# Performance work log

Hardware: AMD Instinct MI355X
Metric: run time of the kernel (lower is better)

The kernel has to match this reference:

```python
import jax, jax.numpy as jnp
import numpy as np

N, E, DIN, H, C = 50000, 800000, 128, 2, 64  # C = hidden_dim*heads (per-head out channels); concat=False -> mean over heads -> layer out dim C
NUM_CLASSES = 4
EPS_GN = 1e-5


def setup_inputs() -> dict:
    key = jax.random.key(0)

    def rn(i, shape, scale):
        return (jax.random.normal(jax.random.fold_in(key, i), shape) * scale).astype(jnp.float32)

    inp = {
        "x": rn(0, (N, DIN), 1.0),
        "edge_index": jax.random.randint(jax.random.fold_in(key, 1), (2, E), 0, N, dtype=jnp.int32),
    }
    layer_in = [DIN, C]
    for li, din in enumerate(layer_in, 1):
        s = 1.0 / np.sqrt(din)
        base = 10 * li
        inp[f"Wl{li}"] = rn(base + 0, (din, H * C), s)
        inp[f"bl{li}"] = jnp.zeros((H * C,), jnp.float32)
        inp[f"Wr{li}"] = rn(base + 1, (din, H * C), s)
        inp[f"br{li}"] = jnp.zeros((H * C,), jnp.float32)
        inp[f"att{li}"] = rn(base + 2, (H, C), 1.0 / np.sqrt(C))
        inp[f"bias{li}"] = jnp.zeros((C,), jnp.float32)
        inp[f"gng{li}"] = jnp.ones((C,), jnp.float32)   # GraphNorm weight
        inp[f"gnb{li}"] = jnp.zeros((C,), jnp.float32)  # GraphNorm bias
        inp[f"gna{li}"] = jnp.ones((C,), jnp.float32)   # GraphNorm mean_scale
    inp["W1"] = rn(100, (C, NUM_CLASSES), 1.0 / np.sqrt(C))
    inp["b1"] = jnp.zeros((NUM_CLASSES,), jnp.float32)
    return inp


def gatv2_layer(x, src, dst, Wl, bl, Wr, br, att, bias):
    # PyG GATv2Conv, concat=False. x: [N, din]
    n = x.shape[0]
    xl = (x @ Wl + bl).reshape(n, H, C)  # source transform
    xr = (x @ Wr + br).reshape(n, H, C)  # target transform
    m = jax.nn.leaky_relu(xl[src] + xr[dst], negative_slope=0.2)  # [E', H, C]
    e = jnp.einsum('ehc,hc->eh', m, att)                           # [E', H]
    emax = jax.lax.stop_gradient(jax.ops.segment_max(e, dst, num_segments=n))
    ee = jnp.exp(e - emax[dst])
    denom = jax.ops.segment_sum(ee, dst, num_segments=n)
    alpha = ee / (denom[dst] + 1e-16)                              # softmax over in-edges of each target
    out = jax.ops.segment_sum(alpha[:, :, None] * xl[src], dst, num_segments=n)  # [N, H, C]
    return out.mean(axis=1) + bias  # concat=False -> mean over heads


def graph_norm(x, gamma, beta, mean_scale):
    # single-graph GraphNorm: stats over all nodes, per feature
    mean = x.mean(axis=0, keepdims=True)
    xc = x - mean_scale * mean
    var = (xc * xc).mean(axis=0, keepdims=True)
    return gamma * xc * jax.lax.rsqrt(var + EPS_GN) + beta


def reference(x, edge_index,
              Wl1, bl1, Wr1, br1, att1, bias1, gng1, gnb1, gna1,
              Wl2, bl2, Wr2, br2, att2, bias2, gng2, gnb2, gna2,
              W1, b1):
    src, dst = edge_index[0], edge_index[1]
    loops = jnp.arange(N, dtype=src.dtype)  # add_self_loops=True
    src = jnp.concatenate([src, loops])
    dst = jnp.concatenate([dst, loops])

    h = gatv2_layer(x, src, dst, Wl1, bl1, Wr1, br1, att1, bias1)
    h = graph_norm(h, gng1, gnb1, gna1)
    h = gatv2_layer(h, src, dst, Wl2, bl2, Wr2, br2, att2, bias2)
    h = graph_norm(h, gng2, gnb2, gna2)

    logits = h @ W1 + b1  # dropout is identity in eval
    return jax.nn.log_softmax(logits, axis=1)
```

## Files before the change

kernel.cpp:

```cpp
#include <hip/hip_runtime.h>
#include <hip/hip_bf16.h>
#include <math.h>

#define HC   128
#define CCH  64
#define NBK  256

typedef __attribute__((ext_vector_type(8))) short short8;
typedef __attribute__((ext_vector_type(4))) float floatx4;

__device__ __forceinline__ unsigned short f2bf(float f) {
  unsigned u = __float_as_uint(f);
  u += 0x7fffu + ((u >> 16) & 1u);
  return (unsigned short)(u >> 16);
}

__device__ __forceinline__ void unpack8(uint4 u, float* f) {
  f[0] = __uint_as_float(u.x << 16);
  f[1] = __uint_as_float(u.x & 0xffff0000u);
  f[2] = __uint_as_float(u.y << 16);
  f[3] = __uint_as_float(u.y & 0xffff0000u);
  f[4] = __uint_as_float(u.z << 16);
  f[5] = __uint_as_float(u.z & 0xffff0000u);
  f[6] = __uint_as_float(u.w << 16);
  f[7] = __uint_as_float(u.w & 0xffff0000u);
}

template <int CTRL>
__device__ __forceinline__ float dpp_add(float x) {
  int t = __builtin_amdgcn_update_dpp(0, __float_as_int(x), CTRL, 0xf, 0xf, true);
  return x + __int_as_float(t);
}

template <int K>
__device__ __forceinline__ void gemm32rows(
    const unsigned short* __restrict__ A,
    const unsigned short* __restrict__ Wlt, const unsigned short* __restrict__ Wrt,
    const float* __restrict__ bl, const float* __restrict__ br,
    unsigned short* __restrict__ xlb, unsigned short* __restrict__ xrb,
    int M, int row0, int tid) {
  const int w = tid >> 6;
  const int lane = tid & 63;
  const bool isR = w >= 2;
  const unsigned short* Wt = isR ? Wrt : Wlt;
  const float* bias = isR ? br : bl;
  unsigned short* out = isR ? xrb : xlb;
  const int col0 = (w & 1) * 64;
  const int mrow = lane & 15, quad = lane >> 4;
  const unsigned short* pa0 = A + (size_t)(row0 + mrow) * K + quad * 8;
  const unsigned short* pa1 = pa0 + (size_t)16 * K;
  const unsigned short* pb = Wt + (size_t)(col0 + mrow) * K + quad * 8;
  floatx4 acc[2][4];
#pragma unroll
  for (int gp = 0; gp < 2; gp++)
#pragma unroll
    for (int ct = 0; ct < 4; ct++) acc[gp][ct] = (floatx4){0.f, 0.f, 0.f, 0.f};
#pragma unroll
  for (int k0 = 0; k0 < K; k0 += 32) {
    short8 a0 = *(const short8*)(pa0 + k0);
    short8 a1 = *(const short8*)(pa1 + k0);
    short8 b0 = *(const short8*)(pb + k0);
    short8 b1 = *(const short8*)(pb + 16 * K + k0);
    short8 b2 = *(const short8*)(pb + 32 * K + k0);
    short8 b3 = *(const short8*)(pb + 48 * K + k0);
    acc[0][0] = __builtin_amdgcn_mfma_f32_16x16x32_bf16(a0, b0, acc[0][0], 0, 0, 0);
    acc[1][0] = __builtin_amdgcn_mfma_f32_16x16x32_bf16(a1, b0, acc[1][0], 0, 0, 0);
    acc[0][1] = __builtin_amdgcn_mfma_f32_16x16x32_bf16(a0, b1, acc[0][1], 0, 0, 0);
    acc[1][1] = __builtin_amdgcn_mfma_f32_16x16x32_bf16(a1, b1, acc[1][1], 0, 0, 0);
    acc[0][2] = __builtin_amdgcn_mfma_f32_16x16x32_bf16(a0, b2, acc[0][2], 0, 0, 0);
    acc[1][2] = __builtin_amdgcn_mfma_f32_16x16x32_bf16(a1, b2, acc[1][2], 0, 0, 0);
    acc[0][3] = __builtin_amdgcn_mfma_f32_16x16x32_bf16(a0, b3, acc[0][3], 0, 0, 0);
    acc[1][3] = __builtin_amdgcn_mfma_f32_16x16x32_bf16(a1, b3, acc[1][3], 0, 0, 0);
  }
#pragma unroll
  for (int gp = 0; gp < 2; gp++) {
#pragma unroll
    for (int ct = 0; ct < 4; ct++) {
      int col = col0 + ct * 16 + mrow;
      float bv = bias[col];
#pragma unroll
      for (int r = 0; r < 4; r++) {
        int row = row0 + gp * 16 + quad * 4 + r;
        if (row < M) out[(size_t)row * HC + col] = f2bf(acc[gp][ct][r] + bv);
      }
    }
  }
}

__global__ __launch_bounds__(256) void bin_cast(
    const int* __restrict__ ei, int E, int chunk, int nB,
    int* __restrict__ blkCnt, int* __restrict__ bucketTotal,
    const float* __restrict__ x, unsigned short* __restrict__ xb, int cnt4,
    const float* __restrict__ Wl, const float* __restrict__ Wr,
    unsigned short* __restrict__ Wlt, unsigned short* __restrict__ Wrt) {
  if ((int)blockIdx.x < NBK) {
    __shared__ int cnt[512];
    for (int j = threadIdx.x; j < nB; j += 256) cnt[j] = 0;
    __syncthreads();
    int e0 = blockIdx.x * chunk;
    int e1 = e0 + chunk; e1 = e1 < E ? e1 : E;
    int e = e0 + threadIdx.x;
    for (; e + 768 < e1; e += 1024) {
      int d0 = __builtin_nontemporal_load(ei + E + e);
      int d1 = __builtin_nontemporal_load(ei + E + e + 256);
      int d2 = __builtin_nontemporal_load(ei + E + e + 512);
      int d3 = __builtin_nontemporal_load(ei + E + e + 768);
      atomicAdd(&cnt[d0 >> 7], 1);
      atomicAdd(&cnt[d1 >> 7], 1);
      atomicAdd(&cnt[d2 >> 7], 1);
      atomicAdd(&cnt[d3 >> 7], 1);
    }
    for (; e < e1; e += 256) {
      int dst = __builtin_nontemporal_load(ei + E + e);
      atomicAdd(&cnt[dst >> 7], 1);
    }
    __syncthreads();
    for (int j = threadIdx.x; j < nB; j += 256) {
      int c = cnt[j];
      blkCnt[blockIdx.x * nB + j] = c;
      if (c) atomicAdd(&bucketTotal[j], c);
    }
  } else {
    int gid = (blockIdx.x - NBK) * 256 + threadIdx.x;
    if (gid < 32768) {
      int sel = gid >> 14;
      int i = gid & 16383;
      int nn = i >> 7, k = i & 127;
      const float* W = sel ? Wr : Wl;
      unsigned short* Wt = sel ? Wrt : Wlt;
      Wt[i] = f2bf(W[k * HC + nn]);
    }
    if (gid >= cnt4) return;
    float4 v = ((const float4*)x)[gid];
    ushort4 o;
    o.x = f2bf(v.x); o.y = f2bf(v.y); o.z = f2bf(v.z); o.w = f2bf(v.w);
    ((ushort4*)xb)[gid] = o;
  }
}

__global__ __launch_bounds__(256) void scan_offsets(
    const int* __restrict__ bucketTotal, int* __restrict__ bucketBase,
    int* __restrict__ blkCnt, int nB, int E) {
  const int j = blockIdx.x;
  const int tid = threadIdx.x;
  __shared__ int red[256];
  __shared__ int col[NBK];
  int s = 0;
  for (int k = tid; k < j; k += 256) s += bucketTotal[k];
  red[tid] = s;
  __syncthreads();
  for (int off = 128; off > 0; off >>= 1) {
    if (tid < off) red[tid] += red[tid + off];
    __syncthreads();
  }
  const int base_j = red[0];
  if (tid == 0) {
    bucketBase[j] = base_j;
    if (j == 0) bucketBase[nB] = E;
  }
  int v = 0;
  if (tid < NBK) { v = blkCnt[tid * nB + j]; col[tid] = v; }
  __syncthreads();
  for (int off = 1; off < NBK; off <<= 1) {
    int t = 0;
    if (tid < NBK && tid >= off) t = col[tid - off];
    __syncthreads();
    if (tid < NBK) col[tid] += t;
    __syncthreads();
  }
  if (tid < NBK) blkCnt[tid * nB + j] = base_j + col[tid] - v;
}

__global__ __launch_bounds__(256) void place_gemm1(
    const int* __restrict__ ei, int E, int chunk, int nB,
    const int* __restrict__ blkCnt, unsigned* __restrict__ ebuf,
    const unsigned short* __restrict__ A,
    const unsigned short* __restrict__ Wlt, const unsigned short* __restrict__ Wrt,
    const float* __restrict__ bl, const float* __restrict__ br,
    unsigned short* __restrict__ xlb, unsigned short* __restrict__ xrb, int M) {
  if ((int)blockIdx.x < NBK) {
    __shared__ int cur[512];
    for (int j = threadIdx.x; j < nB; j += 256)
      cur[j] = blkCnt[blockIdx.x * nB + j];
    __syncthreads();
    int e0 = blockIdx.x * chunk;
    int e1 = e0 + chunk; e1 = e1 < E ? e1 : E;
    int e = e0 + threadIdx.x;
    for (; e + 768 < e1; e += 1024) {
      int d0 = __builtin_nontemporal_load(ei + E + e);
      int d1 = __builtin_nontemporal_load(ei + E + e + 256);
      int d2 = __builtin_nontemporal_load(ei + E + e + 512);
      int d3 = __builtin_nontemporal_load(ei + E + e + 768);
      int s0 = __builtin_nontemporal_load(ei + e);
      int s1 = __builtin_nontemporal_load(ei + e + 256);
      int s2 = __builtin_nontemporal_load(ei + e + 512);
      int s3 = __builtin_nontemporal_load(ei + e + 768);
      int p0 = atomicAdd(&cur[d0 >> 7], 1);
      int p1 = atomicAdd(&cur[d1 >> 7], 1);
      int p2 = atomicAdd(&cur[d2 >> 7], 1);
      int p3 = atomicAdd(&cur[d3 >> 7], 1);
      ebuf[p0] = (unsigned)s0 | ((unsigned)(d0 & 127) << 16);
      ebuf[p1] = (unsigned)s1 | ((unsigned)(d1 & 127) << 16);
      ebuf[p2] = (unsigned)s2 | ((unsigned)(d2 & 127) << 16);
      ebuf[p3] = (unsigned)s3 | ((unsigned)(d3 & 127) << 16);
    }
    for (; e < e1; e += 256) {
      int dst = __builtin_nontemporal_load(ei + E + e);
      int src = __builtin_nontemporal_load(ei + e);
      int pos = atomicAdd(&cur[dst >> 7], 1);
      ebuf[pos] = (unsigned)src | ((unsigned)(dst & 127) << 16);
    }
  } else {
    const int row0 = (blockIdx.x - NBK) * 32;
    if (row0 >= M) return;
    gemm32rows<128>(A, Wlt, Wrt, bl, br, xlb, xrb, M, row0, threadIdx.x);
  }
}

__global__ __launch_bounds__(256) void csr_build(
    const unsigned* __restrict__ ebuf, const int* __restrict__ bucketBase,
    int* __restrict__ row_start, int* __restrict__ deg,
    int* __restrict__ csr_src, int N, int EPtot) {
  const int b = blockIdx.x;
  const int tid = threadIdx.x;
  const int node0 = b * 128;
  const int nb = (N - node0) < 128 ? (N - node0) : 128;
  const int ebase = bucketBase[b];
  const int eend = bucketBase[b + 1];
  __shared__ int degL[128], scanL[128], curL[128];
  if (tid < 128) degL[tid] = 0;
  __syncthreads();
  for (int e = ebase + tid; e < eend; e += 256)
    atomicAdd(&degL[(ebuf[e] >> 16) & 127], 1);
  __syncthreads();
  if (tid < 128) scanL[tid] = degL[tid];
  __syncthreads();
  for (int off = 1; off < 128; off <<= 1) {
    int t = 0;
    if (tid < 128 && tid >= off) t = scanL[tid - off];
    __syncthreads();
    if (tid < 128) scanL[tid] += t;
    __syncthreads();
  }
  if (tid < 128) {
    int rs = ebase + (scanL[tid] - degL[tid]) + node0 + tid;
    curL[tid] = rs;
    if (tid < nb) {
      row_start[node0 + tid] = rs;
      deg[node0 + tid] = degL[tid];
    }
  }
  __syncthreads();
  for (int e = ebase + tid; e < eend; e += 256) {
    unsigned p = ebuf[e];
    int pos = atomicAdd(&curL[(p >> 16) & 127], 1);
    csr_src[pos] = (int)(p & 0xffffu);
  }
  __syncthreads();
  if (tid < nb) csr_src[curL[tid]] = node0 + tid;
  if (b == 0 && tid < 32) csr_src[EPtot + tid] = 0;
}

template <int K>
__global__ __launch_bounds__(256) void gemm_mfma(
    const unsigned short* __restrict__ A,
    const unsigned short* __restrict__ Wlt, const unsigned short* __restrict__ Wrt,
    const float* __restrict__ bl, const float* __restrict__ br,
    unsigned short* __restrict__ xlb, unsigned short* __restrict__ xrb, int M) {
  const int row0 = blockIdx.x * 32;
  if (row0 >= M) return;
  gemm32rows<K>(A, Wlt, Wrt, bl, br, xlb, xrb, M, row0, threadIdx.x);
}

__global__ __launch_bounds__(256) void node_attn(
    const unsigned short* __restrict__ xlb, const unsigned short* __restrict__ xrb,
    const int* __restrict__ csr_src, const int* __restrict__ row_start,
    const int* __restrict__ deg, const float* __restrict__ att,
    const float* __restrict__ bias, unsigned short* __restrict__ outb, int n) {
  int wave = (blockIdx.x * blockDim.x + threadIdx.x) >> 6;
  if (wave >= n) return;
  const int node = wave;
  const int lane = threadIdx.x & 63;
  const int g = lane >> 4;
  const int hl = lane & 15;
  const int c8 = hl << 3;

  float r[8], a[8];
  {
    uint4 u = *(const uint4*)(xrb + (size_t)node * HC + c8);
    unpack8(u, r);
    float4 a0 = *(const float4*)(att + c8);
    float4 a1 = *(const float4*)(att + c8 + 4);
    const float L2E = 1.44269504f;
    a[0] = a0.x * L2E; a[1] = a0.y * L2E; a[2] = a0.z * L2E; a[3] = a0.w * L2E;
    a[4] = a1.x * L2E; a[5] = a1.y * L2E; a[6] = a1.z * L2E; a[7] = a1.w * L2E;
  }

  const int p0 = row_start[node];
  const int pend = p0 + deg[node] + 1;

  float d = 0.f;
  float acc[8] = {0.f, 0.f, 0.f, 0.f, 0.f, 0.f, 0.f, 0.f};

  int s0 = __builtin_nontemporal_load(csr_src + p0 + g);
  uint4 A0 = *(const uint4*)(xlb + (size_t)s0 * HC + c8);
  int s1 = __builtin_nontemporal_load(csr_src + p0 + 4 + g);
  uint4 A1 = *(const uint4*)(xlb + (size_t)s1 * HC + c8);
  int s2 = __builtin_nontemporal_load(csr_src + p0 + 8 + g);
  uint4 A2 = *(const uint4*)(xlb + (size_t)s2 * HC + c8);

  for (int p = p0; p < pend; p += 4) {
    int s3 = __builtin_nontemporal_load(csr_src + p + 12 + g);
    uint4 A3 = *(const uint4*)(xlb + (size_t)s3 * HC + c8);

    float v[8];
    unpack8(A0, v);
    float e1 = 0.f, e2 = 0.f;
#pragma unroll
    for (int i = 0; i < 8; i++) {
      float s = v[i] + r[i];
      e1 = fmaf(a[i], s, e1);
      e2 = fmaf(a[i], fabsf(s), e2);
    }
    float e = fmaf(0.4f, e2, 0.6f * e1);
    e = dpp_add<0xB1>(e);
    e = dpp_add<0x4E>(e);
    e = dpp_add<0x141>(e);

    bool valid = (p + g) < pend;
    float w = valid ? exp2f(e) : 0.f;
    d += w;
#pragma unroll
    for (int i = 0; i < 8; i++) acc[i] = fmaf(w, v[i], acc[i]);
    A0 = A1; A1 = A2; A2 = A3;
  }

#pragma unroll
  for (int ofs = 16; ofs <= 32; ofs <<= 1) {
    d += __shfl_xor(d, ofs);
#pragma unroll
    for (int i = 0; i < 8; i++) acc[i] += __shfl_xor(acc[i], ofs);
  }
  float inv = 1.f / (d + 1e-16f);
  const float* bb = bias + (c8 & 63);
  float o[8];
#pragma unroll
  for (int i = 0; i < 8; i++) {
    float t = acc[i] * inv;
    float t2 = __shfl_xor(t, 8);
    o[i] = 0.5f * (t + t2) + bb[i];
  }
  if (lane < 8) {
    uint4 ou;
    ou.x = (unsigned)f2bf(o[0]) | ((unsigned)f2bf(o[1]) << 16);
    ou.y = (unsigned)f2bf(o[2]) | ((unsigned)f2bf(o[3]) << 16);
    ou.z = (unsigned)f2bf(o[4]) | ((unsigned)f2bf(o[5]) << 16);
    ou.w = (unsigned)f2bf(o[6]) | ((unsigned)f2bf(o[7]) << 16);
    *(uint4*)(outb + (size_t)node * CCH + c8) = ou;
  }
}

__global__ __launch_bounds__(256) void gn_stats(
    const unsigned short* __restrict__ y, float* __restrict__ S, int n) {
  __shared__ float l1a[256], l1b[256], l2a[256], l2b[256];
  int half = threadIdx.x & 31;
  int sub = threadIdx.x >> 5;
  float s1a = 0.f, s1b = 0.f, s2a = 0.f, s2b = 0.f;
  int stride = gridDim.x * 8;
  for (int r = blockIdx.x * 8 + sub; r < n; r += stride) {
    unsigned u = ((const unsigned*)(y + (size_t)r * CCH))[half];
    float va = __uint_as_float(u << 16);
    float vb = __uint_as_float(u & 0xffff0000u);
    s1a += va; s2a = fmaf(va, va, s2a);
    s1b += vb; s2b = fmaf(vb, vb, s2b);
  }
  l1a[threadIdx.x] = s1a; l1b[threadIdx.x] = s1b;
  l2a[threadIdx.x] = s2a; l2b[threadIdx.x] = s2b;
  __syncthreads();
  if (threadIdx.x < 32) {
#pragma unroll
    for (int k = 1; k < 8; k++) {
      s1a += l1a[threadIdx.x + 32 * k];
      s1b += l1b[threadIdx.x + 32 * k];
      s2a += l2a[threadIdx.x + 32 * k];
      s2b += l2b[threadIdx.x + 32 * k];
    }
    atomicAdd(&S[2 * half], s1a);
    atomicAdd(&S[2 * half + 1], s1b);
    atomicAdd(&S[64 + 2 * half], s2a);
    atomicAdd(&S[64 + 2 * half + 1], s2b);
  }
}

__global__ __launch_bounds__(256) void gn_stats_prep(
    const unsigned short* __restrict__ y, float* __restrict__ S,
    int* __restrict__ done, const float* __restrict__ gamma,
    const float* __restrict__ beta, const float* __restrict__ mscale,
    const float* __restrict__ Wl2, const float* __restrict__ bl2,
    const float* __restrict__ Wr2, const float* __restrict__ br2,
    unsigned short* __restrict__ Wl2tb, float* __restrict__ bl2p,
    unsigned short* __restrict__ Wr2tb, float* __restrict__ br2p, int n) {
  __shared__ float l1a[256], l1b[256], l2a[256], l2b[256];
  int half = threadIdx.x & 31;
  int sub = threadIdx.x >> 5;
  float s1a = 0.f, s1b = 0.f, s2a = 0.f, s2b = 0.f;
  int stride = gridDim.x * 8;
  for (int r = blockIdx.x * 8 + sub; r < n; r += stride) {
    unsigned u = ((const unsigned*)(y + (size_t)r * CCH))[half];
    float va = __uint_as_float(u << 16);
    float vb = __uint_as_float(u & 0xffff0000u);
    s1a += va; s2a = fmaf(va, va, s2a);
    s1b += vb; s2b = fmaf(vb, vb, s2b);
  }
  l1a[threadIdx.x] = s1a; l1b[threadIdx.x] = s1b;
  l2a[threadIdx.x] = s2a; l2b[threadIdx.x] = s2b;
  __syncthreads();
  if (threadIdx.x < 32) {
#pragma unroll
    for (int k = 1; k < 8; k++) {
      s1a += l1a[threadIdx.x + 32 * k];
      s1b += l1b[threadIdx.x + 32 * k];
      s2a += l2a[threadIdx.x + 32 * k];
      s2b += l2b[threadIdx.x + 32 * k];
    }
    atomicAdd(&S[2 * half], s1a);
    atomicAdd(&S[2 * half + 1], s1b);
    atomicAdd(&S[64 + 2 * half], s2a);
    atomicAdd(&S[64 + 2 * half + 1], s2b);
  }
  __threadfence();
  __shared__ int isLast;
  if (threadIdx.x == 0) {
    int old = atomicAdd(done, 1);
    isLast = (old == (int)gridDim.x - 1) ? 1 : 0;
  }
  __syncthreads();
  if (!isLast) return;
  __threadfence();
  __shared__ float As[64], Bs[64];
  int t = threadIdx.x;
  if (t < 64) {
    float invn = 1.f / (float)n;
    float mu = S[t] * invn;
    float ms = mscale[t];
    float var = S[64 + t] * invn - 2.f * ms * mu * mu + ms * ms * mu * mu;
    float A = gamma[t] * rsqrtf(var + 1e-5f);
    As[t] = A;
    Bs[t] = beta[t] - A * ms * mu;
  }
  __syncthreads();
  const int side = t >> 7, col = t & 127;
  const float* W = side ? Wr2 : Wl2;
  unsigned short* Wt = side ? Wr2tb : Wl2tb;
  const float* bin = side ? br2 : bl2;
  float* bout = side ? br2p : bl2p;
  float s = 0.f;
  for (int c = 0; c < 64; c++) {
    float w = W[c * HC + col];
    Wt[col * 64 + c] = f2bf(As[c] * w);
    s = fmaf(Bs[c], w, s);
  }
  bout[col] = bin[col] + s;
}

__global__ __launch_bounds__(256) void classify(
    const unsigned short* __restrict__ h,
    const float* __restrict__ S, const float* __restrict__ gamma,
    const float* __restrict__ beta, const float* __restrict__ mscale,
    const float* __restrict__ W, const float* __restrict__ b,
    float* __restrict__ out, int n) {
  __shared__ float4 sW[64];
  __shared__ float sBt[256];
  __shared__ float sb[4];
  int tid = threadIdx.x;
  if (tid < 64) {
    float invn = 1.f / (float)n;
    float mu = S[tid] * invn;
    float ms = mscale[tid];
    float var = S[64 + tid] * invn - 2.f * ms * mu * mu + ms * ms * mu * mu;
    float A = gamma[tid] * rsqrtf(var + 1e-5f);
    float B = beta[tid] - A * ms * mu;
    float4 w = ((const float4*)W)[tid];
    sW[tid] = make_float4(A * w.x, A * w.y, A * w.z, A * w.w);
    sBt[tid * 4 + 0] = B * w.x; sBt[tid * 4 + 1] = B * w.y;
    sBt[tid * 4 + 2] = B * w.z; sBt[tid * 4 + 3] = B * w.w;
  }
  __syncthreads();
  if (tid < 4) {
    float s = b[tid];
    for (int c = 0; c < 64; c++) s += sBt[c * 4 + tid];
    sb[tid] = s;
  }
  __syncthreads();
  int node = blockIdx.x * 256 + tid;
  if (node >= n) return;
  float acc0 = sb[0], acc1 = sb[1], acc2 = sb[2], acc3 = sb[3];
  const uint4* row = (const uint4*)(h + (size_t)node * CCH);
#pragma unroll
  for (int k4 = 0; k4 < 8; k4++) {
    uint4 u = row[k4];
    float v[8];
    unpack8(u, v);
#pragma unroll
    for (int j = 0; j < 8; j++) {
      float4 w = sW[k4 * 8 + j];
      acc0 = fmaf(v[j], w.x, acc0);
      acc1 = fmaf(v[j], w.y, acc1);
      acc2 = fmaf(v[j], w.z, acc2);
      acc3 = fmaf(v[j], w.w, acc3);
    }
  }
  float mx = fmaxf(fmaxf(acc0, acc1), fmaxf(acc2, acc3));
  float s = __expf(acc0 - mx) + __expf(acc1 - mx) + __expf(acc2 - mx) + __expf(acc3 - mx);
  float lse = mx + logf(s);
  float4 o = make_float4(acc0 - lse, acc1 - lse, acc2 - lse, acc3 - lse);
  *((float4*)(out + (size_t)node * 4)) = o;
}

extern "C" void kernel_launch(void* const* d_in, const int* in_sizes, int n_in,
                              void* d_out, int out_size, void* d_ws, size_t ws_size,
                              hipStream_t stream) {
  const float* x     = (const float*)d_in[0];
  const int*   ei    = (const int*)d_in[1];
  const float* Wl1   = (const float*)d_in[2];
  const float* bl1   = (const float*)d_in[3];
  const float* Wr1   = (const float*)d_in[4];
  const float* br1   = (const float*)d_in[5];
  const float* att1  = (const float*)d_in[6];
  const float* bias1 = (const float*)d_in[7];
  const float* gng1  = (const float*)d_in[8];
  const float* gnb1  = (const float*)d_in[9];
  const float* gna1  = (const float*)d_in[10];
  const float* Wl2   = (const float*)d_in[11];
  const float* bl2   = (const float*)d_in[12];
  const float* Wr2   = (const float*)d_in[13];
  const float* br2   = (const float*)d_in[14];
  const float* att2  = (const float*)d_in[15];
  const float* bias2 = (const float*)d_in[16];
  const float* gng2  = (const float*)d_in[17];
  const float* gnb2  = (const float*)d_in[18];
  const float* gna2  = (const float*)d_in[19];
  const float* W1    = (const float*)d_in[20];
  const float* b1    = (const float*)d_in[21];

  const int N = in_sizes[0] / 128;
  const int E = in_sizes[1] / 2;
  const int EP = E + N;
  const int nB = (N + 127) >> 7;
  const int chunk = (E + NBK - 1) / NBK;

  int* bucketTotal = (int*)d_ws;
  float* S1  = (float*)(bucketTotal + 512);
  float* S2  = S1 + 128;
  int* done  = (int*)(S2 + 128);
  float* bl2p = (float*)(done + 64);
  float* br2p = bl2p + 128;
  unsigned short* xb    = (unsigned short*)(br2p + 128);
  unsigned short* xlb   = xb + (size_t)N * HC;
  unsigned short* xrb   = xlb + (size_t)N * HC;
  unsigned short* aggb  = xrb + (size_t)N * HC;
  unsigned short* Wl1tb = aggb + (size_t)N * CCH;
  unsigned short* Wr1tb = Wl1tb + HC * HC;
  unsigned short* Wl2tb = Wr1tb + HC * HC;
  unsigned short* Wr2tb = Wl2tb + HC * CCH;
  int* bucketBase = (int*)(Wr2tb + HC * CCH);
  int* blkCnt  = bucketBase + 512 + 8;
  int* row_st  = blkCnt + NBK * 512;
  int* deg     = row_st + N;
  unsigned* ebuf = (unsigned*)(deg + N);
  int* csr_src = (int*)(ebuf + E);

  dim3 b256(256);
  const int gNode = (N * 64 + 255) / 256;
  const int gCls  = (N + 255) / 256;
  const int gCast = (N * 32 + 255) / 256;
  const int gGemm = (N + 31) / 32;

  hipMemsetAsync(d_ws, 0, 4096, stream);

  bin_cast<<<NBK + gCast, b256, 0, stream>>>(
      ei, E, chunk, nB, blkCnt, bucketTotal,
      x, xb, N * 32, Wl1, Wr1, Wl1tb, Wr1tb);

  scan_offsets<<<nB, b256, 0, stream>>>(bucketTotal, bucketBase, blkCnt, nB, E);

  place_gemm1<<<NBK + gGemm, b256, 0, stream>>>(
      ei, E, chunk, nB, blkCnt, ebuf,
      xb, Wl1tb, Wr1tb, bl1, br1, xlb, xrb, N);

  csr_build<<<nB, b256, 0, stream>>>(ebuf, bucketBase, row_st, deg, csr_src, N, EP);

  node_attn<<<gNode, b256, 0, stream>>>(xlb, xrb, csr_src, row_st, deg, att1, bias1, aggb, N);
  gn_stats_prep<<<256, b256, 0, stream>>>(aggb, S1, done, gng1, gnb1, gna1,
                                          Wl2, bl2, Wr2, br2,
                                          Wl2tb, bl2p, Wr2tb, br2p, N);

  gemm_mfma<64><<<gGemm, b256, 0, stream>>>(aggb, Wl2tb, Wr2tb, bl2p, br2p, xlb, xrb, N);
  node_attn<<<gNode, b256, 0, stream>>>(xlb, xrb, csr_src, row_st, deg, att2, bias2, aggb, N);
  gn_stats<<<256, b256, 0, stream>>>(aggb, S2, N);

  classify<<<gCls, b256, 0, stream>>>(aggb, S2, gng2, gnb2, gna2, W1, b1,
                                      (float*)d_out, N);
}
```

Measured before the change: 327.0 us.

## Widen GEMM tiles to 64 rows, fold classifier prep into stats kernel

The bf16 MFMA GEMM helper now computes 64 rows per block instead of 32, so each loaded weight fragment is reused across twice as many rows and the grid is halved. csr_build is launched with 512 threads to spread its edge loops over more threads. The GraphNorm-to-linear folding that every classify block used to recompute now runs once, in the last block of the stats kernel, using a completion counter. Classify then reads the folded weights and runs with 128-thread blocks. The larger GEMM tile raises register use and lowers the number of blocks, and the last-block pattern adds an atomic and fences.

```diff
diff --git a/kernel.cpp b/kernel.cpp
--- a/kernel.cpp
+++ b/kernel.cpp
@@ -33,7 +33,7 @@
 }
 
 template <int K>
-__device__ __forceinline__ void gemm32rows(
+__device__ __forceinline__ void gemm64rows(
     const unsigned short* __restrict__ A,
     const unsigned short* __restrict__ Wlt, const unsigned short* __restrict__ Wrt,
     const float* __restrict__ bl, const float* __restrict__ br,
@@ -47,33 +47,42 @@
   unsigned short* out = isR ? xrb : xlb;
   const int col0 = (w & 1) * 64;
   const int mrow = lane & 15, quad = lane >> 4;
-  const unsigned short* pa0 = A + (size_t)(row0 + mrow) * K + quad * 8;
-  const unsigned short* pa1 = pa0 + (size_t)16 * K;
+  const unsigned short* pa = A + (size_t)(row0 + mrow) * K + quad * 8;
   const unsigned short* pb = Wt + (size_t)(col0 + mrow) * K + quad * 8;
-  floatx4 acc[2][4];
-#pragma unroll
-  for (int gp = 0; gp < 2; gp++)
+  floatx4 acc[4][4];
+#pragma unroll
+  for (int gp = 0; gp < 4; gp++)
 #pragma unroll
     for (int ct = 0; ct < 4; ct++) acc[gp][ct] = (floatx4){0.f, 0.f, 0.f, 0.f};
 #pragma unroll
   for (int k0 = 0; k0 < K; k0 += 32) {
-    short8 a0 = *(const short8*)(pa0 + k0);
-    short8 a1 = *(const short8*)(pa1 + k0);
+    short8 a0 = *(const short8*)(pa + k0);
+    short8 a1 = *(const short8*)(pa + 16 * K + k0);
+    short8 a2 = *(const short8*)(pa + 32 * K + k0);
+    short8 a3 = *(const short8*)(pa + 48 * K + k0);
     short8 b0 = *(const short8*)(pb + k0);
     short8 b1 = *(const short8*)(pb + 16 * K + k0);
     short8 b2 = *(const short8*)(pb + 32 * K + k0);
     short8 b3 = *(const short8*)(pb + 48 * K + k0);
     acc[0][0] = __builtin_amdgcn_mfma_f32_16x16x32_bf16(a0, b0, acc[0][0], 0, 0, 0);
     acc[1][0] = __builtin_amdgcn_mfma_f32_16x16x32_bf16(a1, b0, acc[1][0], 0, 0, 0);
+    acc[2][0] = __builtin_amdgcn_mfma_f32_16x16x32_bf16(a2, b0, acc[2][0], 0, 0, 0);
+    acc[3][0] = __builtin_amdgcn_mfma_f32_16x16x32_bf16(a3, b0, acc[3][0], 0, 0, 0);
     acc[0][1] = __builtin_amdgcn_mfma_f32_16x16x32_bf16(a0, b1, acc[0][1], 0, 0, 0);
     acc[1][1] = __builtin_amdgcn_mfma_f32_16x16x32_bf16(a1, b1, acc[1][1], 0, 0, 0);
+    acc[2][1] = __builtin_amdgcn_mfma_f32_16x16x32_bf16(a2, b1, acc[2][1], 0, 0, 0);
+    acc[3][1] = __builtin_amdgcn_mfma_f32_16x16x32_bf16(a3, b1, acc[3][1], 0, 0, 0);
     acc[0][2] = __builtin_amdgcn_mfma_f32_16x16x32_bf16(a0, b2, acc[0][2], 0, 0, 0);
     acc[1][2] = __builtin_amdgcn_mfma_f32_16x16x32_bf16(a1, b2, acc[1][2], 0, 0, 0);
+    acc[2][2] = __builtin_amdgcn_mfma_f32_16x16x32_bf16(a2, b2, acc[2][2], 0, 0, 0);
+    acc[3][2] = __builtin_amdgcn_mfma_f32_16x16x32_bf16(a3, b2, acc[3][2], 0, 0, 0);
     acc[0][3] = __builtin_amdgcn_mfma_f32_16x16x32_bf16(a0, b3, acc[0][3], 0, 0, 0);
     acc[1][3] = __builtin_amdgcn_mfma_f32_16x16x32_bf16(a1, b3, acc[1][3], 0, 0, 0);
-  }
-#pragma unroll
-  for (int gp = 0; gp < 2; gp++) {
+    acc[2][3] = __builtin_amdgcn_mfma_f32_16x16x32_bf16(a2, b3, acc[2][3], 0, 0, 0);
+    acc[3][3] = __builtin_amdgcn_mfma_f32_16x16x32_bf16(a3, b3, acc[3][3], 0, 0, 0);
+  }
+#pragma unroll
+  for (int gp = 0; gp < 4; gp++) {
 #pragma unroll
     for (int ct = 0; ct < 4; ct++) {
       int col = col0 + ct * 16 + mrow;
@@ -211,13 +220,13 @@
       ebuf[pos] = (unsigned)src | ((unsigned)(dst & 127) << 16);
     }
   } else {
-    const int row0 = (blockIdx.x - NBK) * 32;
+    const int row0 = (blockIdx.x - NBK) * 64;
     if (row0 >= M) return;
-    gemm32rows<128>(A, Wlt, Wrt, bl, br, xlb, xrb, M, row0, threadIdx.x);
-  }
-}
-
-__global__ __launch_bounds__(256) void csr_build(
+    gemm64rows<128>(A, Wlt, Wrt, bl, br, xlb, xrb, M, row0, threadIdx.x);
+  }
+}
+
+__global__ __launch_bounds__(512) void csr_build(
     const unsigned* __restrict__ ebuf, const int* __restrict__ bucketBase,
     int* __restrict__ row_start, int* __restrict__ deg,
     int* __restrict__ csr_src, int N, int EPtot) {
@@ -230,7 +239,7 @@
   __shared__ int degL[128], scanL[128], curL[128];
   if (tid < 128) degL[tid] = 0;
   __syncthreads();
-  for (int e = ebase + tid; e < eend; e += 256)
+  for (int e = ebase + tid; e < eend; e += 512)
     atomicAdd(&degL[(ebuf[e] >> 16) & 127], 1);
   __syncthreads();
   if (tid < 128) scanL[tid] = degL[tid];
@@ -251,7 +260,7 @@
     }
   }
   __syncthreads();
-  for (int e = ebase + tid; e < eend; e += 256) {
+  for (int e = ebase + tid; e < eend; e += 512) {
     unsigned p = ebuf[e];
     int pos = atomicAdd(&curL[(p >> 16) & 127], 1);
     csr_src[pos] = (int)(p & 0xffffu);
@@ -267,9 +276,9 @@
     const unsigned short* __restrict__ Wlt, const unsigned short* __restrict__ Wrt,
     const float* __restrict__ bl, const float* __restrict__ br,
     unsigned short* __restrict__ xlb, unsigned short* __restrict__ xrb, int M) {
-  const int row0 = blockIdx.x * 32;
+  const int row0 = blockIdx.x * 64;
   if (row0 >= M) return;
-  gemm32rows<K>(A, Wlt, Wrt, bl, br, xlb, xrb, M, row0, threadIdx.x);
+  gemm64rows<K>(A, Wlt, Wrt, bl, br, xlb, xrb, M, row0, threadIdx.x);
 }
 
 __global__ __launch_bounds__(256) void node_attn(
@@ -360,8 +369,12 @@
   }
 }
 
-__global__ __launch_bounds__(256) void gn_stats(
-    const unsigned short* __restrict__ y, float* __restrict__ S, int n) {
+__global__ __launch_bounds__(256) void gn_stats_fold(
+    const unsigned short* __restrict__ y, float* __restrict__ S,
+    int* __restrict__ done2, const float* __restrict__ gamma,
+    const float* __restrict__ beta, const float* __restrict__ mscale,
+    const float* __restrict__ W, const float* __restrict__ b,
+    float* __restrict__ sWf, float* __restrict__ sbf, int n) {
   __shared__ float l1a[256], l1b[256], l2a[256], l2b[256];
   int half = threadIdx.x & 31;
   int sub = threadIdx.x >> 5;
@@ -389,6 +402,35 @@
     atomicAdd(&S[2 * half + 1], s1b);
     atomicAdd(&S[64 + 2 * half], s2a);
     atomicAdd(&S[64 + 2 * half + 1], s2b);
+  }
+  __threadfence();
+  __shared__ int isLast;
+  if (threadIdx.x == 0) {
+    int old = atomicAdd(done2, 1);
+    isLast = (old == (int)gridDim.x - 1) ? 1 : 0;
+  }
+  __syncthreads();
+  if (!isLast) return;
+  __threadfence();
+  __shared__ float sBt[256];
+  int t = threadIdx.x;
+  if (t < 64) {
+    float invn = 1.f / (float)n;
+    float mu = S[t] * invn;
+    float ms = mscale[t];
+    float var = S[64 + t] * invn - 2.f * ms * mu * mu + ms * ms * mu * mu;
+    float A = gamma[t] * rsqrtf(var + 1e-5f);
+    float B = beta[t] - A * ms * mu;
+    float4 w = ((const float4*)W)[t];
+    ((float4*)sWf)[t] = make_float4(A * w.x, A * w.y, A * w.z, A * w.w);
+    sBt[t * 4 + 0] = B * w.x; sBt[t * 4 + 1] = B * w.y;
+    sBt[t * 4 + 2] = B * w.z; sBt[t * 4 + 3] = B * w.w;
+  }
+  __syncthreads();
+  if (t < 4) {
+    float s = b[t];
+    for (int c = 0; c < 64; c++) s += sBt[c * 4 + t];
+    sbf[t] = s;
   }
 }
 
@@ -463,36 +505,17 @@
   bout[col] = bin[col] + s;
 }
 
-__global__ __launch_bounds__(256) void classify(
+__global__ __launch_bounds__(128) void classify(
     const unsigned short* __restrict__ h,
-    const float* __restrict__ S, const float* __restrict__ gamma,
-    const float* __restrict__ beta, const float* __restrict__ mscale,
-    const float* __restrict__ W, const float* __restrict__ b,
+    const float* __restrict__ sWf, const float* __restrict__ sbf,
     float* __restrict__ out, int n) {
   __shared__ float4 sW[64];
-  __shared__ float sBt[256];
   __shared__ float sb[4];
   int tid = threadIdx.x;
-  if (tid < 64) {
-    float invn = 1.f / (float)n;
-    float mu = S[tid] * invn;
-    float ms = mscale[tid];
-    float var = S[64 + tid] * invn - 2.f * ms * mu * mu + ms * ms * mu * mu;
-    float A = gamma[tid] * rsqrtf(var + 1e-5f);
-    float B = beta[tid] - A * ms * mu;
-    float4 w = ((const float4*)W)[tid];
-    sW[tid] = make_float4(A * w.x, A * w.y, A * w.z, A * w.w);
-    sBt[tid * 4 + 0] = B * w.x; sBt[tid * 4 + 1] = B * w.y;
-    sBt[tid * 4 + 2] = B * w.z; sBt[tid * 4 + 3] = B * w.w;
-  }
-  __syncthreads();
-  if (tid < 4) {
-    float s = b[tid];
-    for (int c = 0; c < 64; c++) s += sBt[c * 4 + tid];
-    sb[tid] = s;
-  }
-  __syncthreads();
-  int node = blockIdx.x * 256 + tid;
+  if (tid < 64) sW[tid] = ((const float4*)sWf)[tid];
+  if (tid < 4) sb[tid] = sbf[tid];
+  __syncthreads();
+  int node = blockIdx.x * 128 + tid;
   if (node >= n) return;
   float acc0 = sb[0], acc1 = sb[1], acc2 = sb[2], acc3 = sb[3];
   const uint4* row = (const uint4*)(h + (size_t)node * CCH);
@@ -555,7 +578,9 @@
   int* done  = (int*)(S2 + 128);
   float* bl2p = (float*)(done + 64);
   float* br2p = bl2p + 128;
-  unsigned short* xb    = (unsigned short*)(br2p + 128);
+  float* sWf  = br2p + 128;
+  float* sbf  = sWf + 256;
+  unsigned short* xb    = (unsigned short*)(sbf + 64);
   unsigned short* xlb   = xb + (size_t)N * HC;
   unsigned short* xrb   = xlb + (size_t)N * HC;
   unsigned short* aggb  = xrb + (size_t)N * HC;
@@ -572,9 +597,9 @@
 
   dim3 b256(256);
   const int gNode = (N * 64 + 255) / 256;
-  const int gCls  = (N + 255) / 256;
+  const int gCls  = (N + 127) / 128;
   const int gCast = (N * 32 + 255) / 256;
-  const int gGemm = (N + 31) / 32;
+  const int gGemm = (N + 63) / 64;
 
   hipMemsetAsync(d_ws, 0, 4096, stream);
 
@@ -588,7 +613,7 @@
       ei, E, chunk, nB, blkCnt, ebuf,
       xb, Wl1tb, Wr1tb, bl1, br1, xlb, xrb, N);
 
-  csr_build<<<nB, b256, 0, stream>>>(ebuf, bucketBase, row_st, deg, csr_src, N, EP);
+  csr_build<<<nB, dim3(512), 0, stream>>>(ebuf, bucketBase, row_st, deg, csr_src, N, EP);
 
   node_attn<<<gNode, b256, 0, stream>>>(xlb, xrb, csr_src, row_st, deg, att1, bias1, aggb, N);
   gn_stats_prep<<<256, b256, 0, stream>>>(aggb, S1, done, gng1, gnb1, gna1,
@@ -597,8 +622,8 @@
 
   gemm_mfma<64><<<gGemm, b256, 0, stream>>>(aggb, Wl2tb, Wr2tb, bl2p, br2p, xlb, xrb, N);
   node_attn<<<gNode, b256, 0, stream>>>(xlb, xrb, csr_src, row_st, deg, att2, bias2, aggb, N);
-  gn_stats<<<256, b256, 0, stream>>>(aggb, S2, N);
-
-  classify<<<gCls, b256, 0, stream>>>(aggb, S2, gng2, gnb2, gna2, W1, b1,
-                                      (float*)d_out, N);
-}
+  gn_stats_fold<<<256, b256, 0, stream>>>(aggb, S2, done + 1, gng2, gnb2, gna2,
+                                          W1, b1, sWf, sbf, N);
+
+  classify<<<gCls, dim3(128), 0, stream>>>(aggb, sWf, sbf, (float*)d_out, N);
+}
```

Result: slower. 335.4 us (+2.6%).
